# Performance work log

Hardware: AMD Instinct MI355X
Metric: run time of the kernel (lower is better)

Reference implementation:

```python
import jax, jax.numpy as jnp
import numpy as np

B, N, DIM, H = 4, 1024, 384, 12
EPS = 1e-6


def setup_inputs() -> dict:
    key = jax.random.key(0)
    ks = jax.random.split(key, 5)
    return {
        "x": jax.random.normal(ks[0], (B, N, DIM), dtype=jnp.float32),
        "w_qkv": jax.random.normal(ks[1], (DIM, 3 * DIM), dtype=jnp.float32) * 0.05,
        "w_out": jax.random.normal(ks[2], (DIM, DIM), dtype=jnp.float32) * 0.05,
        "b_out": jax.random.normal(ks[3], (DIM,), dtype=jnp.float32) * 0.05,
        "toeplitz_w": jax.random.normal(ks[4], (2 * N - 1,), dtype=jnp.float32),
    }


def reference(x, w_qkv, w_out, b_out, toeplitz_w):
    b, n, c = x.shape
    d = c // H
    qkv = x @ w_qkv                                   # [B,N,3C]
    q, k, v = jnp.split(qkv, 3, axis=-1)
    def heads(t):
        return t.reshape(b, n, H, d).transpose(0, 2, 1, 3)  # [B,H,N,d]
    q, k, v = heads(q), heads(k), heads(v)
    q = jax.nn.relu(q) + EPS
    k = jax.nn.relu(k) + EPS
    # outer product kv signal: [B,H,N,d,d]
    kv = k[..., :, None] * v[..., None, :]
    kv_flat = kv.reshape(b * H, n, d * d)
    k_flat = k.reshape(b * H, n, d)
    combined = jnp.concatenate([kv_flat, k_flat], axis=-1)   # [BH,N,d^2+d]
    fft_len = 2 * n
    sig_f = jnp.fft.rfft(combined, n=fft_len, axis=1)        # [BH,N+1,d^2+d] complex
    w_pad = jnp.zeros(fft_len, dtype=x.dtype).at[: 2 * n - 1].set(toeplitz_w)
    w_rolled = jnp.roll(w_pad, -(n - 1))
    w_f = jnp.fft.rfft(w_rolled, n=fft_len)                  # [N+1]
    out_f = sig_f * w_f[None, :, None]
    out_t = jnp.fft.irfft(out_f, n=fft_len, axis=1)[:, :n, :]  # [BH,N,d^2+d]
    kv_conv = out_t[:, :, : d * d].reshape(b, H, n, d, d)
    k_conv = out_t[:, :, d * d:].reshape(b, H, n, d)
    num = jnp.einsum('bhnd,bhndc->bhnc', q, kv_conv)
    den = jnp.einsum('bhnd,bhnd->bhn', q, k_conv)[..., None] + EPS
    out = (num / den).transpose(0, 2, 1, 3).reshape(b, n, c)
    return out @ w_out.T + b_out
```

## Files before the change

kernel.cpp:

```cpp
#include <hip/hip_runtime.h>

#define EPS 1e-6f


__global__ __launch_bounds__(256) void qkv_gemm(const float* __restrict__ x,
                                                const float* __restrict__ w,
                                                float* __restrict__ qw,
                                                float* __restrict__ kw,
                                                float* __restrict__ vw) {
    __shared__ float As[32][68];
    __shared__ float Bs[32][68];
    const int t = threadIdx.x;
    const int m0 = blockIdx.y * 64;
    const int c0 = blockIdx.x * 64;
    const int tx = t & 15, ty = t >> 4;

    float acc[4][4];
#pragma unroll
    for (int i = 0; i < 4; i++)
#pragma unroll
        for (int j = 0; j < 4; j++) acc[i][j] = 0.f;

    for (int k0 = 0; k0 < 384; k0 += 32) {
        __syncthreads();
#pragma unroll
        for (int l = 0; l < 2; l++) {
            int idx = t * 2 + l;
            int r = idx >> 3, c4 = (idx & 7) * 4;
            float4 a = *(const float4*)(x + (size_t)(m0 + r) * 384 + k0 + c4);
            As[c4 + 0][r] = a.x;
            As[c4 + 1][r] = a.y;
            As[c4 + 2][r] = a.z;
            As[c4 + 3][r] = a.w;
        }
#pragma unroll
        for (int l = 0; l < 2; l++) {
            int idx = t * 2 + l;
            int kr = idx >> 4, cc = (idx & 15) * 4;
            *(float4*)&Bs[kr][cc] = *(const float4*)(w + (size_t)(k0 + kr) * 1152 + c0 + cc);
        }
        __syncthreads();
#pragma unroll
        for (int kk = 0; kk < 32; kk++) {
            float4 a = *(float4*)&As[kk][ty * 4];
            float4 bb = *(float4*)&Bs[kk][tx * 4];
            float av[4] = {a.x, a.y, a.z, a.w};
            float bv[4] = {bb.x, bb.y, bb.z, bb.w};
#pragma unroll
            for (int i = 0; i < 4; i++)
#pragma unroll
                for (int j = 0; j < 4; j++) acc[i][j] += av[i] * bv[j];
        }
    }
    const int sec = (c0 + tx * 4) / 384;
    float* dst = (sec == 0) ? qw : (sec == 1) ? kw : vw;
    const int cc0 = c0 + tx * 4 - sec * 384;
    const int h = cc0 >> 5, dd = cc0 & 31;
#pragma unroll
    for (int i = 0; i < 4; i++) {
        int row = m0 + ty * 4 + i;
        int b = row >> 10, n = row & 1023;
        float4 o;
        if (sec < 2) {
            o.x = fmaxf(acc[i][0], 0.f) + EPS;
            o.y = fmaxf(acc[i][1], 0.f) + EPS;
            o.z = fmaxf(acc[i][2], 0.f) + EPS;
            o.w = fmaxf(acc[i][3], 0.f) + EPS;
        } else {
            o = make_float4(acc[i][0], acc[i][1], acc[i][2], acc[i][3]);
        }
        *(float4*)(dst + (size_t)((b * 12 + h) * 1024 + n) * 32 + dd) = o;
    }
}

__global__ __launch_bounds__(256) void toep_attn(const float* __restrict__ q,
                                                 const float* __restrict__ k,
                                                 const float* __restrict__ v,
                                                 const float* __restrict__ tw,
                                                 float* __restrict__ op) {
    const int t = threadIdx.x;
    const int n0 = blockIdx.x * 32;
    const int bh = blockIdx.y;
    const int b = bh / 12, h = bh % 12;
    __shared__ float Qt[32][36];
    __shared__ float Kt[32][68];
    __shared__ float Vs[64][36];
    __shared__ float Ss[32][68];
    __shared__ float Ts[128];

    const float* qb = q + (size_t)bh * 32768;
    const float* kb = k + (size_t)bh * 32768;
    const float* vb = v + (size_t)bh * 32768;

    {
        int r = t >> 3, c4 = (t & 7) * 4;
        float4 a = *(const float4*)(qb + (size_t)(n0 + r) * 32 + c4);
        Qt[c4 + 0][r] = a.x;
        Qt[c4 + 1][r] = a.y;
        Qt[c4 + 2][r] = a.z;
        Qt[c4 + 3][r] = a.w;
    }

    float4 kreg[2], vreg[2];
#pragma unroll
    for (int l = 0; l < 2; l++) {
        int idx = t * 2 + l;
        int r = idx >> 3, c4 = (idx & 7) * 4;
        kreg[l] = *(const float4*)(kb + (size_t)r * 32 + c4);
        vreg[l] = *(const float4*)(vb + idx * 4);
    }
#pragma unroll
    for (int l = 0; l < 2; l++) {
        int idx = t * 2 + l;
        int r = idx >> 3, c4 = (idx & 7) * 4;
        Kt[c4 + 0][r] = kreg[l].x;
        Kt[c4 + 1][r] = kreg[l].y;
        Kt[c4 + 2][r] = kreg[l].z;
        Kt[c4 + 3][r] = kreg[l].w;
        *(float4*)&Vs[r][c4] = vreg[l];
    }
    if (t < 95) Ts[t] = tw[n0 + 960 + t];
    __syncthreads();

    const int sy = t >> 4, sx = t & 15;
    const int pr = t >> 3;
    const int pc = (t & 7) * 4;
    double num[4] = {0, 0, 0, 0};
    double den = 0.0;

    for (int tt = 0; tt < 16; tt++) {
        const int m0 = tt * 64;
        if (tt < 15) {
#pragma unroll
            for (int l = 0; l < 2; l++) {
                int idx = t * 2 + l;
                int r = idx >> 3, c4 = (idx & 7) * 4;
                kreg[l] = *(const float4*)(kb + (size_t)(m0 + 64 + r) * 32 + c4);
                vreg[l] = *(const float4*)(vb + (size_t)(m0 + 64) * 32 + idx * 4);
            }
        }

        float acc[2][4];
#pragma unroll
        for (int i = 0; i < 2; i++)
#pragma unroll
            for (int j = 0; j < 4; j++) acc[i][j] = 0.f;
#pragma unroll
        for (int kk = 0; kk < 32; kk++) {
            float2 qa = *(float2*)&Qt[kk][sy * 2];
            float4 kb4 = *(float4*)&Kt[kk][sx * 4];
            float av[2] = {qa.x, qa.y};
            float bv[4] = {kb4.x, kb4.y, kb4.z, kb4.w};
#pragma unroll
            for (int i = 0; i < 2; i++)
#pragma unroll
                for (int j = 0; j < 4; j++) acc[i][j] += av[i] * bv[j];
        }
#pragma unroll
        for (int i = 0; i < 2; i++) {
            int r = sy * 2 + i;
            float4 srow;
            srow.x = acc[i][0] * Ts[r - sx * 4 + 63];
            srow.y = acc[i][1] * Ts[r - sx * 4 + 62];
            srow.z = acc[i][2] * Ts[r - sx * 4 + 61];
            srow.w = acc[i][3] * Ts[r - sx * 4 + 60];
            *(float4*)&Ss[r][sx * 4] = srow;
        }
        __syncthreads();

        if (tt < 15) {
#pragma unroll
            for (int l = 0; l < 2; l++) {
                int idx = t * 2 + l;
                int r = idx >> 3, c4 = (idx & 7) * 4;
                Kt[c4 + 0][r] = kreg[l].x;
                Kt[c4 + 1][r] = kreg[l].y;
                Kt[c4 + 2][r] = kreg[l].z;
                Kt[c4 + 3][r] = kreg[l].w;
            }
            if (t < 95) Ts[t] = tw[n0 - (m0 + 64) + 960 + t];
        }

#pragma unroll 4
        for (int m = 0; m < 64; m++) {
            double s = (double)Ss[pr][m];
            float4 vv = *(float4*)&Vs[m][pc];
            den += s;
            num[0] += s * (double)vv.x;
            num[1] += s * (double)vv.y;
            num[2] += s * (double)vv.z;
            num[3] += s * (double)vv.w;
        }
        __syncthreads();
        if (tt < 15) {
#pragma unroll
            for (int l = 0; l < 2; l++) {
                int idx = t * 2 + l;
                int r = idx >> 3, c4 = (idx & 7) * 4;
                *(float4*)&Vs[r][c4] = vreg[l];
            }
        }
    }
    double inv = 1.0 / (den + (double)EPS);
    float* o = op + (size_t)((b * 1024) + n0 + pr) * 384 + h * 32 + pc;
    float4 o0 = {(float)(num[0] * inv), (float)(num[1] * inv),
                 (float)(num[2] * inv), (float)(num[3] * inv)};
    *(float4*)o = o0;
}

__global__ __launch_bounds__(256) void out_gemm(const float* __restrict__ a,
                                                const float* __restrict__ w,
                                                const float* __restrict__ bias,
                                                float* __restrict__ out) {
    __shared__ float As[32][68];
    __shared__ float Bs[32][68];
    const int t = threadIdx.x;
    const int m0 = blockIdx.y * 64;
    const int c0 = blockIdx.x * 64;
    const int tx = t & 15, ty = t >> 4;

    float acc[4][4];
#pragma unroll
    for (int i = 0; i < 4; i++)
#pragma unroll
        for (int j = 0; j < 4; j++) acc[i][j] = 0.f;

    for (int k0 = 0; k0 < 384; k0 += 32) {
        __syncthreads();
#pragma unroll
        for (int l = 0; l < 2; l++) {
            int idx = t * 2 + l;
            int r = idx >> 3, c4 = (idx & 7) * 4;
            float4 av = *(const float4*)(a + (size_t)(m0 + r) * 384 + k0 + c4);
            As[c4 + 0][r] = av.x;
            As[c4 + 1][r] = av.y;
            As[c4 + 2][r] = av.z;
            As[c4 + 3][r] = av.w;
        }
#pragma unroll
        for (int l = 0; l < 2; l++) {
            int idx = t * 2 + l;
            int r = idx >> 3, c4 = (idx & 7) * 4;
            float4 wv = *(const float4*)(w + (size_t)(c0 + r) * 384 + k0 + c4);
            Bs[c4 + 0][r] = wv.x;
            Bs[c4 + 1][r] = wv.y;
            Bs[c4 + 2][r] = wv.z;
            Bs[c4 + 3][r] = wv.w;
        }
        __syncthreads();
#pragma unroll
        for (int kk = 0; kk < 32; kk++) {
            float4 a4 = *(float4*)&As[kk][ty * 4];
            float4 b4 = *(float4*)&Bs[kk][tx * 4];
            float av[4] = {a4.x, a4.y, a4.z, a4.w};
            float bv[4] = {b4.x, b4.y, b4.z, b4.w};
#pragma unroll
            for (int i = 0; i < 4; i++)
#pragma unroll
                for (int j = 0; j < 4; j++) acc[i][j] += av[i] * bv[j];
        }
    }
    const int col = c0 + tx * 4;
    float4 bb = *(const float4*)(bias + col);
#pragma unroll
    for (int i = 0; i < 4; i++) {
        int row = m0 + ty * 4 + i;
        float4 o = {acc[i][0] + bb.x, acc[i][1] + bb.y,
                    acc[i][2] + bb.z, acc[i][3] + bb.w};
        *(float4*)(out + (size_t)row * 384 + col) = o;
    }
}

extern "C" void kernel_launch(void* const* d_in, const int* in_sizes, int n_in,
                              void* d_out, int out_size, void* d_ws, size_t ws_size,
                              hipStream_t stream) {
    const float* x     = (const float*)d_in[0];
    const float* w_qkv = (const float*)d_in[1];
    const float* w_out = (const float*)d_in[2];
    const float* b_out = (const float*)d_in[3];
    const float* tw    = (const float*)d_in[4];
    float* out = (float*)d_out;

    float* qw = (float*)d_ws;
    float* kw = qw + 1572864;
    float* vw = kw + 1572864;
    float* op = vw + 1572864;

    qkv_gemm<<<dim3(18, 64), 256, 0, stream>>>(x, w_qkv, qw, kw, vw);
    toep_attn<<<dim3(32, 48), 256, 0, stream>>>(qw, kw, vw, tw, op);
    out_gemm<<<dim3(6, 64), 256, 0, stream>>>(op, w_out, b_out, out);
}
```

Measured before the change: 333.6 us.

## Restructure Toeplitz attention to per-row threads with wave-split key ranges

The toep_attn kernel is rewritten so each thread owns one query row, with q held in registers. The four waves of a block each take every fourth key row, reading k and v straight from global memory at wave-uniform addresses. The LDS tiling of Q/K/V/S and the per-tile barriers are removed, and the block's Toeplitz weight window is loaded into LDS once. Block size grows to 64 queries and per-wave fp64 partial sums are combined serially through LDS. This trades LDS traffic and synchronisation for much higher register pressure (32 double accumulators per thread), lower occupancy and half as many blocks.

```diff
diff --git a/kernel.cpp b/kernel.cpp
--- a/kernel.cpp
+++ b/kernel.cpp
@@ -79,133 +79,88 @@
                                                  const float* __restrict__ tw,
                                                  float* __restrict__ op) {
     const int t = threadIdx.x;
-    const int n0 = blockIdx.x * 32;
+    const int r = t & 63;
+    const int wv = __builtin_amdgcn_readfirstlane(t >> 6);
+    const int n0 = blockIdx.x * 64;
     const int bh = blockIdx.y;
     const int b = bh / 12, h = bh % 12;
-    __shared__ float Qt[32][36];
-    __shared__ float Kt[32][68];
-    __shared__ float Vs[64][36];
-    __shared__ float Ss[32][68];
-    __shared__ float Ts[128];
+
+    __shared__ float Tw[1088];
+    __shared__ double red[64][33];
 
     const float* qb = q + (size_t)bh * 32768;
     const float* kb = k + (size_t)bh * 32768;
     const float* vb = v + (size_t)bh * 32768;
 
+    for (int j = t; j < 1087; j += 256) Tw[j] = tw[n0 + j];
+
+    float qr[32];
+#pragma unroll
+    for (int c = 0; c < 8; c++) {
+        float4 f = *(const float4*)(qb + (size_t)(n0 + r) * 32 + c * 4);
+        qr[c * 4 + 0] = f.x; qr[c * 4 + 1] = f.y;
+        qr[c * 4 + 2] = f.z; qr[c * 4 + 3] = f.w;
+    }
+    __syncthreads();
+
+    double num[32];
+#pragma unroll
+    for (int c = 0; c < 32; c++) num[c] = 0.0;
+    double den = 0.0;
+
+    for (int m = wv; m < 1024; m += 4) {
+        const float* kr = kb + (size_t)m * 32;
+        const float* vr = vb + (size_t)m * 32;
+        float s = 0.f;
+#pragma unroll
+        for (int d = 0; d < 32; d++) s += qr[d] * kr[d];
+        s *= Tw[r - m + 1023];
+        double sd = (double)s;
+        den += sd;
+#pragma unroll
+        for (int c = 0; c < 32; c++) num[c] += sd * (double)vr[c];
+    }
+
+    if (wv == 0) {
+#pragma unroll
+        for (int c = 0; c < 32; c++) red[r][c] = num[c];
+        red[r][32] = den;
+    }
+    __syncthreads();
+    if (wv == 1) {
+#pragma unroll
+        for (int c = 0; c < 32; c++) red[r][c] += num[c];
+        red[r][32] += den;
+    }
+    __syncthreads();
+    if (wv == 2) {
+#pragma unroll
+        for (int c = 0; c < 32; c++) red[r][c] += num[c];
+        red[r][32] += den;
+    }
+    __syncthreads();
+    if (wv == 3) {
+#pragma unroll
+        for (int c = 0; c < 32; c++) red[r][c] += num[c];
+        red[r][32] += den;
+    }
+    __syncthreads();
+
     {
-        int r = t >> 3, c4 = (t & 7) * 4;
-        float4 a = *(const float4*)(qb + (size_t)(n0 + r) * 32 + c4);
-        Qt[c4 + 0][r] = a.x;
-        Qt[c4 + 1][r] = a.y;
-        Qt[c4 + 2][r] = a.z;
-        Qt[c4 + 3][r] = a.w;
-    }
-
-    float4 kreg[2], vreg[2];
-#pragma unroll
-    for (int l = 0; l < 2; l++) {
-        int idx = t * 2 + l;
-        int r = idx >> 3, c4 = (idx & 7) * 4;
-        kreg[l] = *(const float4*)(kb + (size_t)r * 32 + c4);
-        vreg[l] = *(const float4*)(vb + idx * 4);
-    }
-#pragma unroll
-    for (int l = 0; l < 2; l++) {
-        int idx = t * 2 + l;
-        int r = idx >> 3, c4 = (idx & 7) * 4;
-        Kt[c4 + 0][r] = kreg[l].x;
-        Kt[c4 + 1][r] = kreg[l].y;
-        Kt[c4 + 2][r] = kreg[l].z;
-        Kt[c4 + 3][r] = kreg[l].w;
-        *(float4*)&Vs[r][c4] = vreg[l];
-    }
-    if (t < 95) Ts[t] = tw[n0 + 960 + t];
-    __syncthreads();
-
-    const int sy = t >> 4, sx = t & 15;
-    const int pr = t >> 3;
-    const int pc = (t & 7) * 4;
-    double num[4] = {0, 0, 0, 0};
-    double den = 0.0;
-
-    for (int tt = 0; tt < 16; tt++) {
-        const int m0 = tt * 64;
-        if (tt < 15) {
-#pragma unroll
-            for (int l = 0; l < 2; l++) {
-                int idx = t * 2 + l;
-                int r = idx >> 3, c4 = (idx & 7) * 4;
-                kreg[l] = *(const float4*)(kb + (size_t)(m0 + 64 + r) * 32 + c4);
-                vreg[l] = *(const float4*)(vb + (size_t)(m0 + 64) * 32 + idx * 4);
-            }
-        }
-
-        float acc[2][4];
-#pragma unroll
-        for (int i = 0; i < 2; i++)
-#pragma unroll
-            for (int j = 0; j < 4; j++) acc[i][j] = 0.f;
-#pragma unroll
-        for (int kk = 0; kk < 32; kk++) {
-            float2 qa = *(float2*)&Qt[kk][sy * 2];
-            float4 kb4 = *(float4*)&Kt[kk][sx * 4];
-            float av[2] = {qa.x, qa.y};
-            float bv[4] = {kb4.x, kb4.y, kb4.z, kb4.w};
-#pragma unroll
-            for (int i = 0; i < 2; i++)
-#pragma unroll
-                for (int j = 0; j < 4; j++) acc[i][j] += av[i] * bv[j];
-        }
-#pragma unroll
-        for (int i = 0; i < 2; i++) {
-            int r = sy * 2 + i;
-            float4 srow;
-            srow.x = acc[i][0] * Ts[r - sx * 4 + 63];
-            srow.y = acc[i][1] * Ts[r - sx * 4 + 62];
-            srow.z = acc[i][2] * Ts[r - sx * 4 + 61];
-            srow.w = acc[i][3] * Ts[r - sx * 4 + 60];
-            *(float4*)&Ss[r][sx * 4] = srow;
-        }
-        __syncthreads();
-
-        if (tt < 15) {
-#pragma unroll
-            for (int l = 0; l < 2; l++) {
-                int idx = t * 2 + l;
-                int r = idx >> 3, c4 = (idx & 7) * 4;
-                Kt[c4 + 0][r] = kreg[l].x;
-                Kt[c4 + 1][r] = kreg[l].y;
-                Kt[c4 + 2][r] = kreg[l].z;
-                Kt[c4 + 3][r] = kreg[l].w;
-            }
-            if (t < 95) Ts[t] = tw[n0 - (m0 + 64) + 960 + t];
-        }
-
-#pragma unroll 4
-        for (int m = 0; m < 64; m++) {
-            double s = (double)Ss[pr][m];
-            float4 vv = *(float4*)&Vs[m][pc];
-            den += s;
-            num[0] += s * (double)vv.x;
-            num[1] += s * (double)vv.y;
-            num[2] += s * (double)vv.z;
-            num[3] += s * (double)vv.w;
-        }
-        __syncthreads();
-        if (tt < 15) {
-#pragma unroll
-            for (int l = 0; l < 2; l++) {
-                int idx = t * 2 + l;
-                int r = idx >> 3, c4 = (idx & 7) * 4;
-                *(float4*)&Vs[r][c4] = vreg[l];
-            }
-        }
-    }
-    double inv = 1.0 / (den + (double)EPS);
-    float* o = op + (size_t)((b * 1024) + n0 + pr) * 384 + h * 32 + pc;
-    float4 o0 = {(float)(num[0] * inv), (float)(num[1] * inv),
-                 (float)(num[2] * inv), (float)(num[3] * inv)};
-    *(float4*)o = o0;
+        double inv = 1.0 / (red[r][32] + (double)EPS);
+        float* o = op + (size_t)(b * 1024 + n0 + r) * 384 + h * 32 + wv * 8;
+        float4 o0, o1;
+        o0.x = (float)(red[r][wv * 8 + 0] * inv);
+        o0.y = (float)(red[r][wv * 8 + 1] * inv);
+        o0.z = (float)(red[r][wv * 8 + 2] * inv);
+        o0.w = (float)(red[r][wv * 8 + 3] * inv);
+        o1.x = (float)(red[r][wv * 8 + 4] * inv);
+        o1.y = (float)(red[r][wv * 8 + 5] * inv);
+        o1.z = (float)(red[r][wv * 8 + 6] * inv);
+        o1.w = (float)(red[r][wv * 8 + 7] * inv);
+        *(float4*)o = o0;
+        *(float4*)(o + 4) = o1;
+    }
 }
 
 __global__ __launch_bounds__(256) void out_gemm(const float* __restrict__ a,
@@ -287,6 +242,6 @@
     float* op = vw + 1572864;
 
     qkv_gemm<<<dim3(18, 64), 256, 0, stream>>>(x, w_qkv, qw, kw, vw);
-    toep_attn<<<dim3(32, 48), 256, 0, stream>>>(qw, kw, vw, tw, op);
+    toep_attn<<<dim3(16, 48), 256, 0, stream>>>(qw, kw, vw, tw, op);
     out_gemm<<<dim3(6, 64), 256, 0, stream>>>(op, w_out, b_out, out);
 }
```

After: 338.3 us. About the same (+1.4%).
